# Kernel optimization log

Measured on AMD Instinct MI355X. Metric: run time of the kernel, lower is better.

## Reference

```python
import math
import jax, jax.numpy as jnp
import numpy as np

B, C, H, W = 8, 512, 32, 32
HEADS = 8


def _mix_rot(re, im, Wm, phi):
    # nn.Linear(dim, dim, bias=False) applied channelwise on [B,C,H,W]:
    # y = x @ Wm.T  ->  einsum over input channel c, output channel d
    re2 = jnp.einsum('bchw,dc->bdhw', re, Wm)
    im2 = jnp.einsum('bchw,dc->bdhw', im, Wm)
    c = jnp.cos(phi)[None, :, None, None]
    s = jnp.sin(phi)[None, :, None, None]
    # complex multiply (re2 + i*im2) * (cos phi + i*sin phi)
    return re2 * c - im2 * s, re2 * s + im2 * c


def setup_inputs() -> dict:
    key = jax.random.key(0)
    ks = jax.random.split(key, 6)
    scale = 1.0 / math.sqrt(C)
    return {
        'z_re': jax.random.normal(ks[0], (B, C, H, W), jnp.float32),
        'z_im': jax.random.normal(ks[1], (B, C, H, W), jnp.float32),
        'Wq': jax.random.normal(ks[2], (C, C), jnp.float32) * scale,
        'phi_q': jnp.zeros((C,), jnp.float32),
        'Wk': jax.random.normal(ks[3], (C, C), jnp.float32) * scale,
        'phi_k': jnp.zeros((C,), jnp.float32),
        'Wv': jax.random.normal(ks[4], (C, C), jnp.float32) * scale,
        'phi_v': jnp.zeros((C,), jnp.float32),
        'Wo': jax.random.normal(ks[5], (C, C), jnp.float32) * scale,
        'phi_o': jnp.zeros((C,), jnp.float32),
    }


def reference(z_re, z_im, Wq, phi_q, Wk, phi_k, Wv, phi_v, Wo, phi_o):
    b, c, h, w = z_re.shape
    T = h * w
    dh = c // HEADS

    def tok(a):  # [B,C,H,W] -> [B,T,C]
        return a.reshape(b, c, T).transpose(0, 2, 1)

    qre, qim = _mix_rot(z_re, z_im, Wq, phi_q)
    kre, kim = _mix_rot(z_re, z_im, Wk, phi_k)
    vre, vim = _mix_rot(z_re, z_im, Wv, phi_v)
    qre, qim = tok(qre), tok(qim)
    kre, kim = tok(kre), tok(kim)
    vre, vim = tok(vre), tok(vim)

    # real part of complex inner product: sums over FULL channel dim (no head split)
    scores = (jnp.einsum('btc,buc->btu', qre, kre)
              + jnp.einsum('btc,buc->btu', qim, kim)) / math.sqrt(dh)
    causal = jnp.triu(jnp.ones((T, T), bool), k=1)
    scores = jnp.where(causal[None], -jnp.inf, scores)
    attn = jax.nn.softmax(scores, axis=-1)

    out_re = jnp.einsum('btu,buc->btc', attn, vre)
    out_im = jnp.einsum('btu,buc->btc', attn, vim)

    def grid(a):  # [B,T,C] -> [B,C,H,W]
        return a.transpose(0, 2, 1).reshape(b, c, h, w)

    return _mix_rot(grid(out_re), grid(out_im), Wo, phi_o)
```

## Files before the change

### kernel.cpp

```cpp
#include <hip/hip_runtime.h>
#include <math.h>

#define NB 8
#define NC 512
#define NT 1024
#define BT (NB * NT)
#define SCALE 0.125f
#define NEG_BIG (-3.0e38f)

typedef __attribute__((ext_vector_type(8))) short short8v;
typedef __attribute__((ext_vector_type(8))) _Float16 half8v;
typedef __attribute__((ext_vector_type(4))) float float4v;
#define MFMA_BF16(A, B, C) __builtin_amdgcn_mfma_f32_16x16x32_bf16(A, B, C, 0, 0, 0)
#define MFMA_F16(A, B, C)  __builtin_amdgcn_mfma_f32_16x16x32_f16(A, B, C, 0, 0, 0)

__device__ __forceinline__ ushort f2bf(float f) {
    union { float f; unsigned int i; } v; v.f = f;
    unsigned int r = v.i + 0x7FFFu + ((v.i >> 16) & 1u);
    return (ushort)(r >> 16);
}

__device__ __forceinline__ ushort f2h(float f) {
    return __builtin_bit_cast(unsigned short, (_Float16)f);
}

__device__ __forceinline__ half8v scale8(short8v raw, float s) {
    half8v h = __builtin_bit_cast(half8v, raw);
    const _Float16 hs = (_Float16)s;
    half8v r;
    #pragma unroll
    for (int q = 0; q < 8; ++q) r[q] = h[q] * hs;
    return r;
}

#if defined(__has_builtin)
#if __has_builtin(__builtin_amdgcn_global_load_lds)
#define HAS_GLDS 1
#endif
#endif

#ifdef HAS_GLDS
__device__ __forceinline__ void glds16(const ushort* g, ushort* l) {
    __builtin_amdgcn_global_load_lds(
        (const __attribute__((address_space(1))) unsigned int*)g,
        (__attribute__((address_space(3))) unsigned int*)l, 16, 0, 0);
}
#endif

template<int ROWS>
__device__ __forceinline__ void stage64(const ushort* __restrict__ g, int rsShorts,
                                        ushort* tile, int w, int lane) {
    const int r8 = lane >> 3;
    const int ck = (lane & 7) ^ r8;
    const ushort* gl = g + (size_t)r8 * rsShorts + (ck << 3);
    constexpr int ni = ROWS / 32;
    #pragma unroll
    for (int s = 0; s < ni; ++s) {
        const int issue = w * ni + s;
#ifdef HAS_GLDS
        glds16(gl + (size_t)issue * 8 * rsShorts, tile + issue * 512);
#else
        const uint4 v = *(const uint4*)(gl + (size_t)issue * 8 * rsShorts);
        *(uint4*)(tile + issue * 512 + lane * 8) = v;
#endif
    }
}

__device__ __forceinline__ short8v frag(const ushort* tile, int rr, int q) {
    return *(const short8v*)(tile + rr * 64 + ((q ^ (rr & 7)) << 3));
}

__device__ __forceinline__ int xcd_swz(int flat, int cpx) {
    return (flat & 7) * cpx + (flat >> 3);
}

__global__ __launch_bounds__(256) void prep_zw_kernel(
    const float* __restrict__ zre, const float* __restrict__ zim,
    ushort* __restrict__ Z,
    const float* __restrict__ Wq, const float* __restrict__ Wk,
    const float* __restrict__ Wv, const float* __restrict__ Wo,
    ushort* __restrict__ Wbf)
{
    const int bx = blockIdx.x;
    const int tid = threadIdx.x;
    if (bx >= 2048) {
        const int idx = (bx - 2048) * 256 + tid;
        const int e4 = idx << 2;
        const int m = e4 >> 18;
        const int off = e4 & ((1 << 18) - 1);
        const float* Ws[4] = {Wq, Wk, Wv, Wo};
        const float4 v = *(const float4*)(Ws[m] + off);
        ushort4 o;
        o.x = f2bf(v.x); o.y = f2bf(v.y); o.z = f2bf(v.z); o.w = f2bf(v.w);
        *(ushort4*)(Wbf + ((size_t)m << 18) + off) = o;
        return;
    }
    const int t0 = (bx & 15) << 6, c0 = ((bx >> 4) & 7) << 6;
    const int bz = bx >> 7, b = bz & 7, comp = bz >> 3;
    const float* src = (comp ? zim : zre) + (size_t)b * NC * NT;
    ushort* dst = Z + (size_t)(comp * NB + b) * NT * NC;

    __shared__ ushort T[64][72];
    #pragma unroll
    for (int r = 0; r < 4; ++r) {
        const int cl = (tid >> 4) + r * 16;
        const int t4 = (tid & 15) << 2;
        const float4 v = *(const float4*)(src + (size_t)(c0 + cl) * NT + t0 + t4);
        T[t4 + 0][cl] = f2bf(v.x); T[t4 + 1][cl] = f2bf(v.y);
        T[t4 + 2][cl] = f2bf(v.z); T[t4 + 3][cl] = f2bf(v.w);
    }
    __syncthreads();
    const int tl = tid >> 2, cc = (tid & 3) << 4;
    ushort* op = dst + (size_t)(t0 + tl) * NC + c0 + cc;
    *(uint4*)op       = *(const uint4*)&T[tl][cc];
    *(uint4*)(op + 8) = *(const uint4*)&T[tl][cc + 8];
}

__global__ __launch_bounds__(256, 2) void proj_qk_kernel(
    const ushort* __restrict__ Z, const ushort* __restrict__ Wbf,
    const float* __restrict__ phiq, const float* __restrict__ phik,
    ushort* __restrict__ qre, ushort* __restrict__ qim,
    ushort* __restrict__ kre, ushort* __restrict__ kim)
{
    const int tid = threadIdx.x;
    const int swz = xcd_swz(blockIdx.x + 64 * blockIdx.y, 64);
    const int d0 = (swz & 7) << 6;
    const int m0 = (swz >> 3) << 7;
    const size_t NE = (size_t)BT * NC;

    __shared__ alignas(16) ushort SM[24576];
    ushort* Zr   = SM;
    ushort* Zi   = SM + 8192;
    ushort* Wq_s = SM + 16384;
    ushort* Wk_s = SM + 20480;
    uint*   R    = (uint*)SM;

    float4v accq[2][4][2] = {};
    float4v acck[2][4][2] = {};

    const int w = tid >> 6, lane = tid & 63;
    const int l15 = lane & 15, quad = lane >> 4;
    const int wm = (w & 1) << 6;
    const int wn = (w >> 1) << 5;

    for (int c0 = 0; c0 < NC; c0 += 64) {
        stage64<128>(Z + (size_t)m0 * NC + c0, NC, Zr, w, lane);
        stage64<128>(Z + NE + (size_t)m0 * NC + c0, NC, Zi, w, lane);
        stage64<64>(Wbf + (size_t)d0 * NC + c0, NC, Wq_s, w, lane);
        stage64<64>(Wbf + ((size_t)1 << 18) + (size_t)d0 * NC + c0, NC, Wk_s, w, lane);
        __syncthreads();
        #pragma unroll
        for (int kk = 0; kk < 2; ++kk) {
            const int q0 = kk * 4 + quad;
            short8v zf[2][4], wqf[2], wkf[2];
            #pragma unroll
            for (int i = 0; i < 4; ++i) {
                zf[0][i] = frag(Zr, wm + i * 16 + l15, q0);
                zf[1][i] = frag(Zi, wm + i * 16 + l15, q0);
            }
            #pragma unroll
            for (int j = 0; j < 2; ++j) {
                wqf[j] = frag(Wq_s, wn + j * 16 + l15, q0);
                wkf[j] = frag(Wk_s, wn + j * 16 + l15, q0);
            }
            #pragma unroll
            for (int c = 0; c < 2; ++c)
                #pragma unroll
                for (int i = 0; i < 4; ++i)
                    #pragma unroll
                    for (int j = 0; j < 2; ++j) {
                        accq[c][i][j] = MFMA_BF16(zf[c][i], wqf[j], accq[c][i][j]);
                        acck[c][i][j] = MFMA_BF16(zf[c][i], wkf[j], acck[c][i][j]);
                    }
        }
        __syncthreads();
    }

    float cq[2], sq[2], ck2[2], sk2[2];
    #pragma unroll
    for (int j = 0; j < 2; ++j) {
        const int d = d0 + wn + j * 16 + l15;
        const float pq = phiq[d], pk = phik[d];
        cq[j] = cosf(pq); sq[j] = sinf(pq);
        ck2[j] = cosf(pk); sk2[j] = sinf(pk);
    }
    const int g = tid >> 4, cl = tid & 15;

    #pragma unroll
    for (int j = 0; j < 2; ++j)
        #pragma unroll
        for (int i = 0; i < 4; ++i)
            #pragma unroll
            for (int r = 0; r < 4; ++r) {
                const int row = wm + i * 16 + quad * 4 + r;
                const int col = wn + j * 16 + l15;
                const float ar = accq[0][i][j][r], ai = accq[1][i][j][r];
                R[row * 76 + col] = (uint)f2bf(ar * cq[j] - ai * sq[j])
                                  | ((uint)f2bf(ar * sq[j] + ai * cq[j]) << 16);
            }
    __syncthreads();
    #pragma unroll
    for (int s = 0; s < 8; ++s) {
        const int row = g * 8 + s;
        const uint4 p = *(const uint4*)&R[row * 76 + cl * 4];
        uint2 re, im;
        re.x = (p.x & 0xFFFFu) | (p.y << 16);
        re.y = (p.z & 0xFFFFu) | (p.w << 16);
        im.x = (p.x >> 16) | (p.y & 0xFFFF0000u);
        im.y = (p.z >> 16) | (p.w & 0xFFFF0000u);
        const size_t off = (size_t)(m0 + row) * NC + d0 + cl * 4;
        *(uint2*)(qre + off) = re;
        *(uint2*)(qim + off) = im;
    }
    __syncthreads();

    #pragma unroll
    for (int j = 0; j < 2; ++j)
        #pragma unroll
        for (int i = 0; i < 4; ++i)
            #pragma unroll
            for (int r = 0; r < 4; ++r) {
                const int row = wm + i * 16 + quad * 4 + r;
                const int col = wn + j * 16 + l15;
                const float br = acck[0][i][j][r], bi = acck[1][i][j][r];
                R[row * 76 + col] = (uint)f2bf(br * ck2[j] - bi * sk2[j])
                                  | ((uint)f2bf(br * sk2[j] + bi * ck2[j]) << 16);
            }
    __syncthreads();
    #pragma unroll
    for (int s = 0; s < 8; ++s) {
        const int row = g * 8 + s;
        const uint4 p = *(const uint4*)&R[row * 76 + cl * 4];
        uint2 re, im;
        re.x = (p.x & 0xFFFFu) | (p.y << 16);
        re.y = (p.z & 0xFFFFu) | (p.w << 16);
        im.x = (p.x >> 16) | (p.y & 0xFFFF0000u);
        im.y = (p.z >> 16) | (p.w & 0xFFFF0000u);
        const size_t off = (size_t)(m0 + row) * NC + d0 + cl * 4;
        *(uint2*)(kre + off) = re;
        *(uint2*)(kim + off) = im;
    }
}

__global__ __launch_bounds__(256, 3) void proj_v_kernel(
    const ushort* __restrict__ Z, const ushort* __restrict__ Wbf,
    const float* __restrict__ phiv,
    ushort* __restrict__ vre, ushort* __restrict__ vim)
{
    const int tid = threadIdx.x;
    const int swz = xcd_swz(blockIdx.x + 4 * blockIdx.y, 64);
    const int d0 = (swz & 3) << 7;
    const int bt0 = (swz >> 2) << 6;
    const size_t NE = (size_t)BT * NC;

    __shared__ alignas(16) ushort SM[19456];
    ushort* Wv_s = SM;
    ushort* Zr   = SM + 8192;
    ushort* Zi   = SM + 12288;
    uint*   R    = (uint*)SM;

    float4v acc[2][4][2] = {};

    const int w = tid >> 6, lane = tid & 63;
    const int l15 = lane & 15, quad = lane >> 4;
    const int wm = (w & 1) << 6;
    const int wn = (w >> 1) << 5;

    for (int c0 = 0; c0 < NC; c0 += 64) {
        stage64<128>(Wbf + ((size_t)2 << 18) + (size_t)d0 * NC + c0, NC, Wv_s, w, lane);
        stage64<64>(Z + (size_t)bt0 * NC + c0, NC, Zr, w, lane);
        stage64<64>(Z + NE + (size_t)bt0 * NC + c0, NC, Zi, w, lane);
        __syncthreads();
        #pragma unroll
        for (int kk = 0; kk < 2; ++kk) {
            const int q0 = kk * 4 + quad;
            short8v wvf[4], zf[2][2];
            #pragma unroll
            for (int i = 0; i < 4; ++i)
                wvf[i] = frag(Wv_s, wm + i * 16 + l15, q0);
            #pragma unroll
            for (int j = 0; j < 2; ++j) {
                zf[0][j] = frag(Zr, wn + j * 16 + l15, q0);
                zf[1][j] = frag(Zi, wn + j * 16 + l15, q0);
            }
            #pragma unroll
            for (int c = 0; c < 2; ++c)
                #pragma unroll
                for (int i = 0; i < 4; ++i)
                    #pragma unroll
                    for (int j = 0; j < 2; ++j)
                        acc[c][i][j] = MFMA_BF16(wvf[i], zf[c][j], acc[c][i][j]);
        }
        __syncthreads();
    }

    const int d_own = d0 + wm + (l15 >> 2) * 16 + quad * 4 + (l15 & 3);
    const float ph_own = phiv[d_own];
    const float c_own = cosf(ph_own), s_own = sinf(ph_own);

    #pragma unroll
    for (int i = 0; i < 4; ++i)
        #pragma unroll
        for (int r = 0; r < 4; ++r) {
            const int src = (lane & 48) | (i * 4 + r);
            const float cs = __shfl(c_own, src, 64);
            const float sn = __shfl(s_own, src, 64);
            const int row = wm + i * 16 + quad * 4 + r;
            #pragma unroll
            for (int j = 0; j < 2; ++j) {
                const int col = wn + j * 16 + l15;
                const float vr = acc[0][i][j][r], vi = acc[1][i][j][r];
                R[row * 76 + col] = (uint)f2h(vr * cs - vi * sn)
                                  | ((uint)f2h(vr * sn + vi * cs) << 16);
            }
        }
    __syncthreads();
    const int g = tid >> 4, cl = tid & 15;
    const int b = bt0 >> 10, t0 = bt0 & 1023;
    #pragma unroll
    for (int s = 0; s < 8; ++s) {
        const int row = g * 8 + s;
        const uint4 p = *(const uint4*)&R[row * 76 + cl * 4];
        uint2 re, im;
        re.x = (p.x & 0xFFFFu) | (p.y << 16);
        re.y = (p.z & 0xFFFFu) | (p.w << 16);
        im.x = (p.x >> 16) | (p.y & 0xFFFF0000u);
        im.y = (p.z >> 16) | (p.w & 0xFFFF0000u);
        const size_t off = (size_t)b * NC * NT + (size_t)(d0 + row) * NT + t0 + cl * 4;
        *(uint2*)(vre + off) = re;
        *(uint2*)(vim + off) = im;
    }
}

__global__ __launch_bounds__(256, 2) void scores_kernel(
    const ushort* __restrict__ qre, const ushort* __restrict__ qim,
    const ushort* __restrict__ kre, const ushort* __restrict__ kim,
    ushort* __restrict__ Pp, float2* __restrict__ stats)
{
    const int swz = xcd_swz(blockIdx.x + 8 * (blockIdx.y + 8 * blockIdx.z), 64);
    const int u0b = (swz & 7) << 7;
    const int t0b = (7 - ((swz >> 3) & 7)) << 7;
    if (u0b > t0b) return;
    const int b = swz >> 6;
    const int tid = threadIdx.x;
    const size_t qb = (size_t)b * NT * NC;

    __shared__ alignas(16) ushort SM[32768];
    ushort* Rs = SM;

    float4v acc[4][4] = {};

    const int w = tid >> 6, lane = tid & 63;
    const int l15 = lane & 15, quad = lane >> 4;
    const int wm = (w & 1) << 6;
    const int wn = (w >> 1) << 6;

    stage64<128>(qre + qb + (size_t)t0b * NC, NC, SM, w, lane);
    stage64<128>(kre + qb + (size_t)u0b * NC, NC, SM + 8192, w, lane);
    __syncthreads();

    for (int s = 0; s < 16; ++s) {
        const int cur = (s & 1) << 14;
        const int nxt = cur ^ 16384;
        if (s + 1 < 16) {
            const int c0n = ((s + 1) >> 1) << 6;
            const ushort* qs = ((s + 1) & 1 ? qim : qre) + qb + (size_t)t0b * NC + c0n;
            const ushort* ks = ((s + 1) & 1 ? kim : kre) + qb + (size_t)u0b * NC + c0n;
            stage64<128>(qs, NC, SM + nxt, w, lane);
            stage64<128>(ks, NC, SM + nxt + 8192, w, lane);
        }
        const ushort* Qs = SM + cur;
        const ushort* Ks = SM + cur + 8192;
        #pragma unroll
        for (int kk = 0; kk < 2; ++kk) {
            const int q0 = kk * 4 + quad;
            short8v qf[4], kf[4];
            #pragma unroll
            for (int i = 0; i < 4; ++i) {
                qf[i] = frag(Qs, wm + i * 16 + l15, q0);
                kf[i] = frag(Ks, wn + i * 16 + l15, q0);
            }
            #pragma unroll
            for (int i = 0; i < 4; ++i)
                #pragma unroll
                for (int j = 0; j < 4; ++j)
                    acc[i][j] = MFMA_BF16(qf[i], kf[j], acc[i][j]);
        }
        __syncthreads();
    }

    const int sub = (u0b + wn) >> 6;
    float2* st = stats + (size_t)(b * 16 + sub) * NT;
    #pragma unroll
    for (int i = 0; i < 4; ++i)
        #pragma unroll
        for (int r = 0; r < 4; ++r) {
            const int t = t0b + wm + i * 16 + quad * 4 + r;
            float v[4]; float m = NEG_BIG;
            #pragma unroll
            for (int j = 0; j < 4; ++j) {
                const int u = u0b + wn + j * 16 + l15;
                const float x = (u > t) ? NEG_BIG : acc[i][j][r] * SCALE;
                v[j] = x; m = fmaxf(m, x);
            }
            #pragma unroll
            for (int d = 1; d < 16; d <<= 1) m = fmaxf(m, __shfl_xor(m, d, 64));
            float l = 0.f;
            const int row = wm + i * 16 + quad * 4 + r;
            #pragma unroll
            for (int j = 0; j < 4; ++j) {
                const float e = __expf(v[j] - m);
                l += e;
                Rs[row * 140 + wn + j * 16 + l15] = f2h(e);
            }
            #pragma unroll
            for (int d = 1; d < 16; d <<= 1) l += __shfl_xor(l, d, 64);
            if (l15 == 0) st[t] = make_float2(m, l);
        }
    __syncthreads();
    ushort* Pb = Pp + (size_t)b * NT * NT;
    const int g = tid >> 5, cl = tid & 31;
    #pragma unroll
    for (int s = 0; s < 16; ++s) {
        const int row = g * 16 + s;
        const uint2 p = *(const uint2*)&Rs[row * 140 + cl * 4];
        *(uint2*)(Pb + (size_t)(t0b + row) * NT + u0b + cl * 4) = p;
    }
}

__global__ __launch_bounds__(256, 2) void pv_kernel(
    const ushort* __restrict__ Pp, const float2* __restrict__ stats,
    const ushort* __restrict__ vre, const ushort* __restrict__ vim,
    ushort* __restrict__ Ore, ushort* __restrict__ Oim)
{
    const int swz = xcd_swz(blockIdx.x + 8 * (blockIdx.y + 8 * blockIdx.z), 64);
    const int c0b = (swz & 7) << 6;
    const int t0b = (7 - ((swz >> 3) & 7)) << 7;
    const int b = swz >> 6;
    const int tid = threadIdx.x;
    const ushort* P = Pp + ((size_t)b * NT + t0b) * NT;
    const size_t vb = (size_t)b * NC * NT;
    const int iters = (t0b + 128) >> 6;

    __shared__ alignas(16) ushort SM[37120];
    float* sLds = (float*)(SM + 32768);
    uint*  R    = (uint*)SM;

    float4v acc[2][4][2] = {};

    const int w = tid >> 6, lane = tid & 63;
    const int l15 = lane & 15, quad = lane >> 4;
    const int wm = (w & 1) << 6;
    const int wn = (w >> 1) << 5;

    stage64<128>(P, NT, SM, w, lane);
    stage64<64>(vre + vb + (size_t)c0b * NT, NT, SM + 8192, w, lane);
    stage64<64>(vim + vb + (size_t)c0b * NT, NT, SM + 12288, w, lane);
    if (tid < 128) {
        const int t = t0b + tid;
        float mv[16], lv[16];
        #pragma unroll
        for (int s = 0; s < 16; ++s) {
            if (s < iters) {
                const float2 v = stats[(size_t)(b * 16 + s) * NT + t];
                mv[s] = v.x; lv[s] = v.y;
            } else { mv[s] = NEG_BIG; lv[s] = 0.f; }
        }
        float M = NEG_BIG;
        #pragma unroll
        for (int s = 0; s < 16; ++s) M = fmaxf(M, mv[s]);
        float L = 0.f; float ev[16];
        #pragma unroll
        for (int s = 0; s < 16; ++s) { ev[s] = __expf(mv[s] - M); L += ev[s] * lv[s]; }
        const float inv = 1.0f / L;
        #pragma unroll
        for (int s = 0; s < 16; ++s) sLds[tid * 17 + s] = ev[s] * inv;
    }
    __syncthreads();

    for (int it = 0; it < iters; ++it) {
        const int cur = (it & 1) << 14;
        const int nxt = cur ^ 16384;
        if (it + 1 < iters) {
            const int u0 = (it + 1) << 6;
            stage64<128>(P + u0, NT, SM + nxt, w, lane);
            stage64<64>(vre + vb + (size_t)c0b * NT + u0, NT, SM + nxt + 8192, w, lane);
            stage64<64>(vim + vb + (size_t)c0b * NT + u0, NT, SM + nxt + 12288, w, lane);
        }
        const ushort* Ps = SM + cur;
        const ushort* Vr = SM + cur + 8192;
        const ushort* Vi = SM + cur + 12288;
        #pragma unroll
        for (int kk = 0; kk < 2; ++kk) {
            const int q0 = kk * 4 + quad;
            half8v pf[4], vf[2][2];
            #pragma unroll
            for (int i = 0; i < 4; ++i) {
                const int row = wm + i * 16 + l15;
                pf[i] = scale8(frag(Ps, row, q0), sLds[row * 17 + it]);
            }
            #pragma unroll
            for (int j = 0; j < 2; ++j) {
                vf[0][j] = __builtin_bit_cast(half8v, frag(Vr, wn + j * 16 + l15, q0));
                vf[1][j] = __builtin_bit_cast(half8v, frag(Vi, wn + j * 16 + l15, q0));
            }
            #pragma unroll
            for (int c = 0; c < 2; ++c)
                #pragma unroll
                for (int i = 0; i < 4; ++i)
                    #pragma unroll
                    for (int j = 0; j < 2; ++j)
                        acc[c][i][j] = MFMA_F16(pf[i], vf[c][j], acc[c][i][j]);
        }
        __syncthreads();
    }

    #pragma unroll
    for (int i = 0; i < 4; ++i)
        #pragma unroll
        for (int j = 0; j < 2; ++j)
            #pragma unroll
            for (int r = 0; r < 4; ++r) {
                const int row = wm + i * 16 + quad * 4 + r;
                const int col = wn + j * 16 + l15;
                R[row * 76 + col] = (uint)f2bf(acc[0][i][j][r])
                                  | ((uint)f2bf(acc[1][i][j][r]) << 16);
            }
    __syncthreads();
    const int g = tid >> 4, cl = tid & 15;
    #pragma unroll
    for (int s = 0; s < 8; ++s) {
        const int row = g * 8 + s;
        const uint4 p = *(const uint4*)&R[row * 76 + cl * 4];
        uint2 re, im;
        re.x = (p.x & 0xFFFFu) | (p.y << 16);
        re.y = (p.z & 0xFFFFu) | (p.w << 16);
        im.x = (p.x >> 16) | (p.y & 0xFFFF0000u);
        im.y = (p.z >> 16) | (p.w & 0xFFFF0000u);
        const size_t off = ((size_t)b * NT + t0b + row) * NC + c0b + cl * 4;
        *(uint2*)(Ore + off) = re;
        *(uint2*)(Oim + off) = im;
    }
}

__global__ __launch_bounds__(256, 3) void proj_out_kernel(
    const ushort* __restrict__ Ore, const ushort* __restrict__ Oim,
    const ushort* __restrict__ Wbf, const float* __restrict__ phio,
    float* __restrict__ outRe, float* __restrict__ outIm)
{
    const int tid = threadIdx.x;
    const int swz = xcd_swz(blockIdx.x + 4 * blockIdx.y, 64);
    const int d0 = (swz & 3) << 7;
    const int bt0 = (swz >> 2) << 6;

    __shared__ alignas(16) ushort SM[19456];
    ushort* Wo_s = SM;
    ushort* Or_s = SM + 8192;
    ushort* Oi_s = SM + 12288;
    float*  Rf   = (float*)SM;

    float4v acc[2][4][2] = {};

    const int w = tid >> 6, lane = tid & 63;
    const int l15 = lane & 15, quad = lane >> 4;
    const int wm = (w & 1) << 6;
    const int wn = (w >> 1) << 5;

    for (int c0 = 0; c0 < NC; c0 += 64) {
        stage64<128>(Wbf + ((size_t)3 << 18) + (size_t)d0 * NC + c0, NC, Wo_s, w, lane);
        stage64<64>(Ore + (size_t)bt0 * NC + c0, NC, Or_s, w, lane);
        stage64<64>(Oim + (size_t)bt0 * NC + c0, NC, Oi_s, w, lane);
        __syncthreads();
        #pragma unroll
        for (int kk = 0; kk < 2; ++kk) {
            const int q0 = kk * 4 + quad;
            short8v wof[4], of[2][2];
            #pragma unroll
            for (int i = 0; i < 4; ++i)
                wof[i] = frag(Wo_s, wm + i * 16 + l15, q0);
            #pragma unroll
            for (int j = 0; j < 2; ++j) {
                of[0][j] = frag(Or_s, wn + j * 16 + l15, q0);
                of[1][j] = frag(Oi_s, wn + j * 16 + l15, q0);
            }
            #pragma unroll
            for (int c = 0; c < 2; ++c)
                #pragma unroll
                for (int i = 0; i < 4; ++i)
                    #pragma unroll
                    for (int j = 0; j < 2; ++j)
                        acc[c][i][j] = MFMA_BF16(wof[i], of[c][j], acc[c][i][j]);
        }
        __syncthreads();
    }

    const int d_own = d0 + wm + (l15 >> 2) * 16 + quad * 4 + (l15 & 3);
    const float ph_own = phio[d_own];
    const float c_own = cosf(ph_own), s_own = sinf(ph_own);
    const int g = tid >> 4, cl = tid & 15;
    const int b = bt0 >> 10, t0 = bt0 & 1023;

    #pragma unroll
    for (int i = 0; i < 4; ++i)
        #pragma unroll
        for (int r = 0; r < 4; ++r) {
            const int src = (lane & 48) | (i * 4 + r);
            const float cs = __shfl(c_own, src, 64);
            const float sn = __shfl(s_own, src, 64);
            const int row = wm + i * 16 + quad * 4 + r;
            #pragma unroll
            for (int j = 0; j < 2; ++j) {
                const int col = wn + j * 16 + l15;
                Rf[row * 76 + col] = acc[0][i][j][r] * cs - acc[1][i][j][r] * sn;
            }
        }
    __syncthreads();
    #pragma unroll
    for (int s = 0; s < 8; ++s) {
        const int row = g * 8 + s;
        const float4 p = *(const float4*)&Rf[row * 76 + cl * 4];
        *(float4*)(outRe + (size_t)b * NC * NT + (size_t)(d0 + row) * NT + t0 + cl * 4) = p;
    }
    __syncthreads();

    #pragma unroll
    for (int i = 0; i < 4; ++i)
        #pragma unroll
        for (int r = 0; r < 4; ++r) {
            const int src = (lane & 48) | (i * 4 + r);
            const float cs = __shfl(c_own, src, 64);
            const float sn = __shfl(s_own, src, 64);
            const int row = wm + i * 16 + quad * 4 + r;
            #pragma unroll
            for (int j = 0; j < 2; ++j) {
                const int col = wn + j * 16 + l15;
                Rf[row * 76 + col] = acc[0][i][j][r] * sn + acc[1][i][j][r] * cs;
            }
        }
    __syncthreads();
    #pragma unroll
    for (int s = 0; s < 8; ++s) {
        const int row = g * 8 + s;
        const float4 p = *(const float4*)&Rf[row * 76 + cl * 4];
        *(float4*)(outIm + (size_t)b * NC * NT + (size_t)(d0 + row) * NT + t0 + cl * 4) = p;
    }
}

extern "C" void kernel_launch(void* const* d_in, const int* in_sizes, int n_in,
                              void* d_out, int out_size, void* d_ws, size_t ws_size,
                              hipStream_t stream) {
    (void)in_sizes; (void)n_in; (void)out_size; (void)ws_size;
    const float* z_re  = (const float*)d_in[0];
    const float* z_im  = (const float*)d_in[1];
    const float* Wq    = (const float*)d_in[2];
    const float* phi_q = (const float*)d_in[3];
    const float* Wk    = (const float*)d_in[4];
    const float* phi_k = (const float*)d_in[5];
    const float* Wv    = (const float*)d_in[6];
    const float* phi_v = (const float*)d_in[7];
    const float* Wo    = (const float*)d_in[8];
    const float* phi_o = (const float*)d_in[9];

    const size_t NE = (size_t)BT * NC;
    ushort* ws  = (ushort*)d_ws;
    ushort* qre = ws + 0 * NE; ushort* qim = ws + 1 * NE;
    ushort* kre = ws + 2 * NE; ushort* kim = ws + 3 * NE;
    ushort* vre = ws + 4 * NE; ushort* vim = ws + 5 * NE;
    ushort* Wbf = ws + 6 * NE;
    ushort* Z  = (ushort*)d_out;
    ushort* Pp = (ushort*)d_out + 2 * NE;
    float2* stats = (float2*)d_out;

    const dim3 blk(256);
    hipLaunchKernelGGL(prep_zw_kernel, dim3(3072), blk, 0, stream,
                       z_re, z_im, Z, Wq, Wk, Wv, Wo, Wbf);
    hipLaunchKernelGGL(proj_qk_kernel, dim3(BT / 128, NC / 64), blk, 0, stream,
                       Z, Wbf, phi_q, phi_k, qre, qim, kre, kim);
    hipLaunchKernelGGL(proj_v_kernel, dim3(NC / 128, BT / 64), blk, 0, stream,
                       Z, Wbf, phi_v, vre, vim);
    hipLaunchKernelGGL(scores_kernel, dim3(NT / 128, NT / 128, NB), blk, 0, stream,
                       qre, qim, kre, kim, Pp, stats);
    hipLaunchKernelGGL(pv_kernel, dim3(NC / 64, NT / 128, NB), blk, 0, stream,
                       Pp, stats, vre, vim, qre, qim);
    hipLaunchKernelGGL(proj_out_kernel, dim3(NC / 128, BT / 64), blk, 0, stream,
                       qre, qim, Wbf, phi_o, (float*)d_out, (float*)d_out + NE);
}
```

Measured before the change: 188.4 us.

## Double-buffer LDS staging in projection GEMM kernels to overlap loads with MFMA

Result: slower. 197.9 us (+5.0%).

```diff
diff --git a/kernel.cpp b/kernel.cpp
--- a/kernel.cpp
+++ b/kernel.cpp
@@ -128,12 +128,8 @@
     const int m0 = (swz >> 3) << 7;
     const size_t NE = (size_t)BT * NC;
 
-    __shared__ alignas(16) ushort SM[24576];
-    ushort* Zr   = SM;
-    ushort* Zi   = SM + 8192;
-    ushort* Wq_s = SM + 16384;
-    ushort* Wk_s = SM + 20480;
-    uint*   R    = (uint*)SM;
+    __shared__ alignas(16) ushort SM[32768];
+    uint* R = (uint*)SM;
 
     float4v accq[2][4][2] = {};
     float4v acck[2][4][2] = {};
@@ -143,35 +139,58 @@
     const int wm = (w & 1) << 6;
     const int wn = (w >> 1) << 5;
 
+    stage64<128>(Z + (size_t)m0 * NC, NC, SM, w, lane);
+    stage64<64>(Wbf + (size_t)d0 * NC, NC, SM + 8192, w, lane);
+    stage64<64>(Wbf + ((size_t)1 << 18) + (size_t)d0 * NC, NC, SM + 12288, w, lane);
+    __syncthreads();
+
     for (int c0 = 0; c0 < NC; c0 += 64) {
-        stage64<128>(Z + (size_t)m0 * NC + c0, NC, Zr, w, lane);
-        stage64<128>(Z + NE + (size_t)m0 * NC + c0, NC, Zi, w, lane);
-        stage64<64>(Wbf + (size_t)d0 * NC + c0, NC, Wq_s, w, lane);
-        stage64<64>(Wbf + ((size_t)1 << 18) + (size_t)d0 * NC + c0, NC, Wk_s, w, lane);
-        __syncthreads();
+        stage64<128>(Z + NE + (size_t)m0 * NC + c0, NC, SM + 16384, w, lane);
+        stage64<64>(Wbf + (size_t)d0 * NC + c0, NC, SM + 24576, w, lane);
+        stage64<64>(Wbf + ((size_t)1 << 18) + (size_t)d0 * NC + c0, NC, SM + 28672, w, lane);
         #pragma unroll
         for (int kk = 0; kk < 2; ++kk) {
             const int q0 = kk * 4 + quad;
-            short8v zf[2][4], wqf[2], wkf[2];
-            #pragma unroll
-            for (int i = 0; i < 4; ++i) {
-                zf[0][i] = frag(Zr, wm + i * 16 + l15, q0);
-                zf[1][i] = frag(Zi, wm + i * 16 + l15, q0);
-            }
+            short8v zf[4], wqf[2], wkf[2];
+            #pragma unroll
+            for (int i = 0; i < 4; ++i) zf[i] = frag(SM, wm + i * 16 + l15, q0);
             #pragma unroll
             for (int j = 0; j < 2; ++j) {
-                wqf[j] = frag(Wq_s, wn + j * 16 + l15, q0);
-                wkf[j] = frag(Wk_s, wn + j * 16 + l15, q0);
-            }
-            #pragma unroll
-            for (int c = 0; c < 2; ++c)
+                wqf[j] = frag(SM + 8192, wn + j * 16 + l15, q0);
+                wkf[j] = frag(SM + 12288, wn + j * 16 + l15, q0);
+            }
+            #pragma unroll
+            for (int i = 0; i < 4; ++i)
                 #pragma unroll
-                for (int i = 0; i < 4; ++i)
-                    #pragma unroll
-                    for (int j = 0; j < 2; ++j) {
-                        accq[c][i][j] = MFMA_BF16(zf[c][i], wqf[j], accq[c][i][j]);
-                        acck[c][i][j] = MFMA_BF16(zf[c][i], wkf[j], acck[c][i][j]);
-                    }
+                for (int j = 0; j < 2; ++j) {
+                    accq[0][i][j] = MFMA_BF16(zf[i], wqf[j], accq[0][i][j]);
+                    acck[0][i][j] = MFMA_BF16(zf[i], wkf[j], acck[0][i][j]);
+                }
+        }
+        __syncthreads();
+        if (c0 + 64 < NC) {
+            stage64<128>(Z + (size_t)m0 * NC + c0 + 64, NC, SM, w, lane);
+            stage64<64>(Wbf + (size_t)d0 * NC + c0 + 64, NC, SM + 8192, w, lane);
+            stage64<64>(Wbf + ((size_t)1 << 18) + (size_t)d0 * NC + c0 + 64, NC, SM + 12288, w, lane);
+        }
+        #pragma unroll
+        for (int kk = 0; kk < 2; ++kk) {
+            const int q0 = kk * 4 + quad;
+            short8v zf[4], wqf[2], wkf[2];
+            #pragma unroll
+            for (int i = 0; i < 4; ++i) zf[i] = frag(SM + 16384, wm + i * 16 + l15, q0);
+            #pragma unroll
+            for (int j = 0; j < 2; ++j) {
+                wqf[j] = frag(SM + 24576, wn + j * 16 + l15, q0);
+                wkf[j] = frag(SM + 28672, wn + j * 16 + l15, q0);
+            }
+            #pragma unroll
+            for (int i = 0; i < 4; ++i)
+                #pragma unroll
+                for (int j = 0; j < 2; ++j) {
+                    accq[1][i][j] = MFMA_BF16(zf[i], wqf[j], accq[1][i][j]);
+                    acck[1][i][j] = MFMA_BF16(zf[i], wkf[j], acck[1][i][j]);
+                }
         }
         __syncthreads();
     }
@@ -242,7 +261,7 @@
     }
 }
 
-__global__ __launch_bounds__(256, 3) void proj_v_kernel(
+__global__ __launch_bounds__(256, 2) void proj_v_kernel(
     const ushort* __restrict__ Z, const ushort* __restrict__ Wbf,
     const float* __restrict__ phiv,
     ushort* __restrict__ vre, ushort* __restrict__ vim)
@@ -253,11 +272,8 @@
     const int bt0 = (swz >> 2) << 6;
     const size_t NE = (size_t)BT * NC;
 
-    __shared__ alignas(16) ushort SM[19456];
-    ushort* Wv_s = SM;
-    ushort* Zr   = SM + 8192;
-    ushort* Zi   = SM + 12288;
-    uint*   R    = (uint*)SM;
+    __shared__ alignas(16) ushort SM[32768];
+    uint* R = (uint*)SM;
 
     float4v acc[2][4][2] = {};
 
@@ -266,11 +282,23 @@
     const int wm = (w & 1) << 6;
     const int wn = (w >> 1) << 5;
 
-    for (int c0 = 0; c0 < NC; c0 += 64) {
-        stage64<128>(Wbf + ((size_t)2 << 18) + (size_t)d0 * NC + c0, NC, Wv_s, w, lane);
-        stage64<64>(Z + (size_t)bt0 * NC + c0, NC, Zr, w, lane);
-        stage64<64>(Z + NE + (size_t)bt0 * NC + c0, NC, Zi, w, lane);
-        __syncthreads();
+    stage64<128>(Wbf + ((size_t)2 << 18) + (size_t)d0 * NC, NC, SM, w, lane);
+    stage64<64>(Z + (size_t)bt0 * NC, NC, SM + 8192, w, lane);
+    stage64<64>(Z + NE + (size_t)bt0 * NC, NC, SM + 12288, w, lane);
+    __syncthreads();
+
+    for (int it = 0; it < 8; ++it) {
+        const int cur = (it & 1) << 14;
+        const int nxt = cur ^ 16384;
+        if (it < 7) {
+            const int c0n = (it + 1) << 6;
+            stage64<128>(Wbf + ((size_t)2 << 18) + (size_t)d0 * NC + c0n, NC, SM + nxt, w, lane);
+            stage64<64>(Z + (size_t)bt0 * NC + c0n, NC, SM + nxt + 8192, w, lane);
+            stage64<64>(Z + NE + (size_t)bt0 * NC + c0n, NC, SM + nxt + 12288, w, lane);
+        }
+        const ushort* Wv_s = SM + cur;
+        const ushort* Zr   = SM + cur + 8192;
+        const ushort* Zi   = SM + cur + 12288;
         #pragma unroll
         for (int kk = 0; kk < 2; ++kk) {
             const int q0 = kk * 4 + quad;
@@ -543,7 +571,7 @@
     }
 }
 
-__global__ __launch_bounds__(256, 3) void proj_out_kernel(
+__global__ __launch_bounds__(256, 2) void proj_out_kernel(
     const ushort* __restrict__ Ore, const ushort* __restrict__ Oim,
     const ushort* __restrict__ Wbf, const float* __restrict__ phio,
     float* __restrict__ outRe, float* __restrict__ outIm)
@@ -553,11 +581,8 @@
     const int d0 = (swz & 3) << 7;
     const int bt0 = (swz >> 2) << 6;
 
-    __shared__ alignas(16) ushort SM[19456];
-    ushort* Wo_s = SM;
-    ushort* Or_s = SM + 8192;
-    ushort* Oi_s = SM + 12288;
-    float*  Rf   = (float*)SM;
+    __shared__ alignas(16) ushort SM[32768];
+    float* Rf = (float*)SM;
 
     float4v acc[2][4][2] = {};
 
@@ -566,11 +591,23 @@
     const int wm = (w & 1) << 6;
     const int wn = (w >> 1) << 5;
 
-    for (int c0 = 0; c0 < NC; c0 += 64) {
-        stage64<128>(Wbf + ((size_t)3 << 18) + (size_t)d0 * NC + c0, NC, Wo_s, w, lane);
-        stage64<64>(Ore + (size_t)bt0 * NC + c0, NC, Or_s, w, lane);
-        stage64<64>(Oim + (size_t)bt0 * NC + c0, NC, Oi_s, w, lane);
-        __syncthreads();
+    stage64<128>(Wbf + ((size_t)3 << 18) + (size_t)d0 * NC, NC, SM, w, lane);
+    stage64<64>(Ore + (size_t)bt0 * NC, NC, SM + 8192, w, lane);
+    stage64<64>(Oim + (size_t)bt0 * NC, NC, SM + 12288, w, lane);
+    __syncthreads();
+
+    for (int it = 0; it < 8; ++it) {
+        const int cur = (it & 1) << 14;
+        const int nxt = cur ^ 16384;
+        if (it < 7) {
+            const int c0n = (it + 1) << 6;
+            stage64<128>(Wbf + ((size_t)3 << 18) + (size_t)d0 * NC + c0n, NC, SM + nxt, w, lane);
+            stage64<64>(Ore + (size_t)bt0 * NC + c0n, NC, SM + nxt + 8192, w, lane);
+            stage64<64>(Oim + (size_t)bt0 * NC + c0n, NC, SM + nxt + 12288, w, lane);
+        }
+        const ushort* Wo_s = SM + cur;
+        const ushort* Or_s = SM + cur + 8192;
+        const ushort* Oi_s = SM + cur + 12288;
         #pragma unroll
         for (int kk = 0; kk < 2; ++kk) {
             const int q0 = kk * 4 + quad;
```
